# Performance work log

Measured on AMD Instinct MI355X. Metric: run time of the kernel, lower is better.

## Reference

```python
import jax, jax.numpy as jnp
import numpy as np

NF4 = jnp.array([-1.0, -0.6961928009986877, -0.5250730514526367, -0.39491748809814453,
                 -0.28444138169288635, -0.18477343022823334, -0.09105003625154495, 0.0,
                 0.07958029955625534, 0.16093020141124725, 0.24611230194568634,
                 0.33791524171829224, 0.44070982933044434, 0.5626170039176941,
                 0.7229568362236023, 1.0], dtype=jnp.float32)
BLOCK_SIZE = 64
SCALING = 32.0 / 16.0  # alpha / rank


def setup_inputs() -> dict:
    key = jax.random.key(0)
    k = jax.random.split(key, 6)
    B, S, IN, OUT, R = 4, 128, 4096, 11008, 16
    n_blocks = (OUT * IN) // BLOCK_SIZE  # 704512, exact (no padding needed)
    return {
        "x": jax.random.normal(k[0], (B, S, IN), jnp.float32),
        "weight_indices": jax.random.randint(k[1], (OUT, IN), 0, 16, dtype=jnp.int32),
        "weight_scales": jax.random.uniform(k[2], (n_blocks,), jnp.float32),
        "lora_A": jax.random.normal(k[3], (IN, R), jnp.float32),
        "lora_B": jax.random.normal(k[4], (R, OUT), jnp.float32),
        "bias": jax.random.normal(k[5], (OUT,), jnp.float32),
    }


def dequantize_nf4(indices, scales, shape):
    # LUT gather then blockwise absmax scale
    w = NF4[indices.reshape(-1)]                    # [out*in]
    w = w.reshape(-1, BLOCK_SIZE) * scales[:, None]  # [n_blocks, block]
    return w.reshape(shape)                          # [out, in]


def reference(x, weight_indices, weight_scales, lora_A, lora_B, bias):
    W = dequantize_nf4(weight_indices, weight_scales, weight_indices.shape)  # [out, in]
    base = jnp.einsum("bsi,oi->bso", x, W) + bias                            # F.linear
    lora = (x @ lora_A) @ lora_B                                             # low-rank path (dropout p=0 -> identity)
    return base + lora * SCALING
```

## Files before the change

### kernel.cpp

```cpp
#include <hip/hip_runtime.h>
#include <stdint.h>

typedef __bf16 bf16x8 __attribute__((ext_vector_type(8)));
typedef float f32x4 __attribute__((ext_vector_type(4)));
typedef unsigned short ushort_t;

#define N_OUT 11008
#define K_DIM 4096
#define M_DIM 512
#define BM 128
#define BN 64
#define BK 64
#define NT 64
#define LDB 72
#define BUF (64 * LDB)

__constant__ float c_nf4[16] = {
    -1.0f, -0.6961928009986877f, -0.5250730514526367f, -0.39491748809814453f,
    -0.28444138169288635f, -0.18477343022823334f, -0.09105003625154495f, 0.0f,
    0.07958029955625534f, 0.16093020141124725f, 0.24611230194568634f,
    0.33791524171829224f, 0.44070982933044434f, 0.5626170039176941f,
    0.7229568362236023f, 1.0f};

__device__ __forceinline__ uint32_t pkbf(float lo, float hi) {
  uint32_t ul = __builtin_bit_cast(uint32_t, lo);
  uint32_t uh = __builtin_bit_cast(uint32_t, hi);
  return ((ul + 0x8000u) >> 16) | ((uh + 0x8000u) & 0xffff0000u);
}

__device__ __forceinline__ bf16x8 ldfrag(const ushort_t* p) {
  uint4 r = *reinterpret_cast<const uint4*>(p);
  return __builtin_bit_cast(bf16x8, r);
}

__device__ __forceinline__ bf16x8 asfrag(uint4 r) {
  return __builtin_bit_cast(bf16x8, r);
}

__device__ __forceinline__ uint32_t dq2(int a, int b, float s, const float2* lut) {
  float2 l = lut[a | (b << 4)];
  return pkbf(l.x * s, l.y * s);
}

__global__ void k_prep(const float* __restrict__ x, const float* __restrict__ lA,
                       const float* __restrict__ lB, ushort_t* __restrict__ xbf,
                       ushort_t* __restrict__ xap, ushort_t* __restrict__ btp) {
  __shared__ float red[16][17];
  const int b = blockIdx.x, t = threadIdx.x;
  if (b < 1024) {
    int oc = b * 256 + t;
    const float4* s4 = reinterpret_cast<const float4*>(x) + (size_t)oc * 2;
    float4 v0 = s4[0], v1 = s4[1];
    uint4 o;
    o.x = pkbf(v0.x, v0.y);
    o.y = pkbf(v0.z, v0.w);
    o.z = pkbf(v1.x, v1.y);
    o.w = pkbf(v1.z, v1.w);
    ((uint4*)xbf)[oc] = o;
  } else if (b < 1536) {
    int m = b - 1024;
    int r = t & 15, part = t >> 4;
    const float* xr = x + (size_t)m * K_DIM + part * 256;
    const float* ar = lA + (size_t)(part * 256) * 16 + r;
    float acc = 0.f;
#pragma unroll 8
    for (int k = 0; k < 256; ++k) acc += xr[k] * ar[(size_t)k * 16];
    red[part][r] = acc;
    __syncthreads();
    if (t < 32) {
      float v = 0.f;
      if (t < 16) {
        for (int p = 0; p < 16; ++p) v += red[p][t];
        v *= 2.0f;
      }
      uint32_t u = __builtin_bit_cast(uint32_t, v);
      xap[(size_t)m * 32 + t] = (ushort_t)((u + 0x8000u) >> 16);
    }
  } else {
    int o = (b - 1536) * 256 + t;
    uint32_t p[8];
#pragma unroll
    for (int j = 0; j < 8; ++j)
      p[j] = pkbf(lB[(size_t)(2 * j) * N_OUT + o], lB[(size_t)(2 * j + 1) * N_OUT + o]);
    uint4* dst = reinterpret_cast<uint4*>(btp + (size_t)o * 32);
    dst[0] = make_uint4(p[0], p[1], p[2], p[3]);
    dst[1] = make_uint4(p[4], p[5], p[6], p[7]);
    dst[2] = make_uint4(0u, 0u, 0u, 0u);
    dst[3] = make_uint4(0u, 0u, 0u, 0u);
  }
}

__launch_bounds__(256, 3)
__global__ void k_main(const ushort_t* __restrict__ xbf, const int* __restrict__ wi,
                       const float* __restrict__ sc, const ushort_t* __restrict__ xap,
                       const ushort_t* __restrict__ btp, const float* __restrict__ bias,
                       float* __restrict__ out) {
  __shared__ __align__(16) ushort_t lds_b[3 * BUF];
  __shared__ float2 lutp[256];

  const int t = threadIdx.x;
  const int lane = t & 63;
  const int w = t >> 6;
  const int q = lane >> 4;
  const int m0 = blockIdx.x * BM;
  const int o0 = blockIdx.y * BN;

  lutp[t] = make_float2(c_nf4[t & 15], c_nf4[t >> 4]);

  const int brow = t >> 2, bq = t & 3;
  const int* gb = wi + (size_t)(o0 + brow) * K_DIM + bq * 16;
  const float* gs = sc + (size_t)(o0 + brow) * 64;
  const int lbo = brow * LDB + bq * 16;

  const ushort_t* gA = xbf + (size_t)(m0 + w * 32 + (lane & 15)) * K_DIM + q * 8;

  f32x4 acc[2][4];
#pragma unroll
  for (int mi = 0; mi < 2; ++mi)
#pragma unroll
    for (int ni = 0; ni < 4; ++ni) acc[mi][ni] = (f32x4){0.f, 0.f, 0.f, 0.f};

  int4 bi[2][4];
  float bs[2];
  uint4 a_reg[2][2];
#pragma unroll
  for (int j = 0; j < 4; ++j) bi[0][j] = reinterpret_cast<const int4*>(gb)[j];
  bs[0] = gs[0];
#pragma unroll
  for (int j = 0; j < 4; ++j) bi[1][j] = reinterpret_cast<const int4*>(gb + 64)[j];
  bs[1] = gs[1];
#pragma unroll
  for (int mi = 0; mi < 2; ++mi)
#pragma unroll
    for (int kc = 0; kc < 2; ++kc)
      a_reg[mi][kc] =
          *reinterpret_cast<const uint4*>(gA + (size_t)mi * 16 * K_DIM + kc * 32);

  __syncthreads();

  {
    ushort_t* lb = lds_b + lbo;
    uint4 w0, w1;
    w0.x = dq2(bi[0][0].x, bi[0][0].y, bs[0], lutp);
    w0.y = dq2(bi[0][0].z, bi[0][0].w, bs[0], lutp);
    w0.z = dq2(bi[0][1].x, bi[0][1].y, bs[0], lutp);
    w0.w = dq2(bi[0][1].z, bi[0][1].w, bs[0], lutp);
    w1.x = dq2(bi[0][2].x, bi[0][2].y, bs[0], lutp);
    w1.y = dq2(bi[0][2].z, bi[0][2].w, bs[0], lutp);
    w1.z = dq2(bi[0][3].x, bi[0][3].y, bs[0], lutp);
    w1.w = dq2(bi[0][3].z, bi[0][3].w, bs[0], lutp);
    *reinterpret_cast<uint4*>(lb) = w0;
    *reinterpret_cast<uint4*>(lb + 8) = w1;
  }
#pragma unroll
  for (int j = 0; j < 4; ++j) bi[0][j] = reinterpret_cast<const int4*>(gb + 128)[j];
  bs[0] = gs[2];

  unsigned off_r = 0, off_w = BUF, off_s = 2 * BUF;

#pragma unroll 2
  for (int kt = 0; kt < NT; ++kt) {
    __syncthreads();
    const ushort_t* bb = lds_b + off_r + (lane & 15) * LDB + q * 8;
    bf16x8 bv0[4], bv1[4];
#pragma unroll
    for (int ni = 0; ni < 4; ++ni) bv0[ni] = ldfrag(bb + ni * 16 * LDB);
#pragma unroll
    for (int ni = 0; ni < 4; ++ni) bv1[ni] = ldfrag(bb + ni * 16 * LDB + 32);
    const int ns = (kt + 1) & 1;
    if (kt + 1 < NT) {
      ushort_t* lb = lds_b + off_w + lbo;
      uint4 w0, w1;
      w0.x = dq2(bi[ns][0].x, bi[ns][0].y, bs[ns], lutp);
      w0.y = dq2(bi[ns][0].z, bi[ns][0].w, bs[ns], lutp);
      w0.z = dq2(bi[ns][1].x, bi[ns][1].y, bs[ns], lutp);
      w0.w = dq2(bi[ns][1].z, bi[ns][1].w, bs[ns], lutp);
      w1.x = dq2(bi[ns][2].x, bi[ns][2].y, bs[ns], lutp);
      w1.y = dq2(bi[ns][2].z, bi[ns][2].w, bs[ns], lutp);
      w1.z = dq2(bi[ns][3].x, bi[ns][3].y, bs[ns], lutp);
      w1.w = dq2(bi[ns][3].z, bi[ns][3].w, bs[ns], lutp);
      *reinterpret_cast<uint4*>(lb) = w0;
      *reinterpret_cast<uint4*>(lb + 8) = w1;
    }
#pragma unroll
    for (int mi = 0; mi < 2; ++mi)
#pragma unroll
      for (int ni = 0; ni < 4; ++ni)
        acc[mi][ni] = __builtin_amdgcn_mfma_f32_16x16x32_bf16(
            asfrag(a_reg[mi][0]), bv0[ni], acc[mi][ni], 0, 0, 0);
#pragma unroll
    for (int mi = 0; mi < 2; ++mi)
#pragma unroll
      for (int ni = 0; ni < 4; ++ni)
        acc[mi][ni] = __builtin_amdgcn_mfma_f32_16x16x32_bf16(
            asfrag(a_reg[mi][1]), bv1[ni], acc[mi][ni], 0, 0, 0);
    if (kt + 3 < NT) {
      const int4* gp = reinterpret_cast<const int4*>(gb + (size_t)(kt + 3) * 64);
#pragma unroll
      for (int j = 0; j < 4; ++j) bi[ns][j] = gp[j];
      bs[ns] = gs[kt + 3];
    }
    if (kt + 1 < NT) {
#pragma unroll
      for (int mi = 0; mi < 2; ++mi)
#pragma unroll
        for (int kc = 0; kc < 2; ++kc)
          a_reg[mi][kc] = *reinterpret_cast<const uint4*>(
              gA + (size_t)mi * 16 * K_DIM + (size_t)(kt + 1) * 64 + kc * 32);
    }
    unsigned tmp = off_r;
    off_r = off_w;
    off_w = off_s;
    off_s = tmp;
  }

  {
    uint4 la[2], lb4[4];
#pragma unroll
    for (int mi = 0; mi < 2; ++mi)
      la[mi] = *reinterpret_cast<const uint4*>(
          xap + (size_t)(m0 + w * 32 + mi * 16 + (lane & 15)) * 32 + q * 8);
#pragma unroll
    for (int ni = 0; ni < 4; ++ni)
      lb4[ni] = *reinterpret_cast<const uint4*>(
          btp + (size_t)(o0 + ni * 16 + (lane & 15)) * 32 + q * 8);
#pragma unroll
    for (int mi = 0; mi < 2; ++mi)
#pragma unroll
      for (int ni = 0; ni < 4; ++ni)
        acc[mi][ni] = __builtin_amdgcn_mfma_f32_16x16x32_bf16(
            asfrag(la[mi]), asfrag(lb4[ni]), acc[mi][ni], 0, 0, 0);
  }

  const int cl = lane & 15, rg = q * 4;
#pragma unroll
  for (int ni = 0; ni < 4; ++ni) {
    int col = o0 + ni * 16 + cl;
    float bvs = bias[col];
#pragma unroll
    for (int mi = 0; mi < 2; ++mi) {
      int row0 = m0 + w * 32 + mi * 16 + rg;
      float* op = out + (size_t)row0 * N_OUT + col;
#pragma unroll
      for (int i = 0; i < 4; ++i) op[(size_t)i * N_OUT] = acc[mi][ni][i] + bvs;
    }
  }
}

extern "C" void kernel_launch(void* const* d_in, const int* in_sizes, int n_in,
                              void* d_out, int out_size, void* d_ws, size_t ws_size,
                              hipStream_t stream) {
  const float* x = (const float*)d_in[0];
  const int* wi = (const int*)d_in[1];
  const float* sc = (const float*)d_in[2];
  const float* lA = (const float*)d_in[3];
  const float* lB = (const float*)d_in[4];
  const float* bias = (const float*)d_in[5];
  float* out = (float*)d_out;

  char* wsb = (char*)d_ws;
  ushort_t* xbf = (ushort_t*)wsb;
  ushort_t* xap = (ushort_t*)(wsb + (4u << 20));
  ushort_t* btp = (ushort_t*)(wsb + (4u << 20) + (32u << 10));

  k_prep<<<1579, 256, 0, stream>>>(x, lA, lB, xbf, xap, btp);
  dim3 grid(M_DIM / BM, N_OUT / BN);
  k_main<<<grid, 256, 0, stream>>>(xbf, wi, sc, xap, btp, bias, out);
}
```

Measured before the change: 408.9 us.

## Remap grid for XCD L2 reuse and dequantize NF4 with register byte-permutes

Replaces the 2D grid with a 1D grid of 704 blocks remapped so that the four M-tiles sharing a weight column tile land on the same XCD. Those blocks can then share the int32 weight indices in that XCD's L2 instead of each fetching them separately; blocks whose remapped index falls past the last tile exit early. NF4 dequantization no longer reads a float2 pair LUT in LDS. Each thread builds a per-block scaled bf16 table in registers and looks values up with v_perm byte selects. The LDS ring shrinks from triple to double buffering, and B-fragment loads are split into two phases to reduce register pressure. The trade-off is a few idle blocks and more ALU work to build the table at every k-step.

```diff
diff --git a/kernel.cpp b/kernel.cpp
--- a/kernel.cpp
+++ b/kernel.cpp
@@ -37,9 +37,42 @@
   return __builtin_bit_cast(bf16x8, r);
 }
 
-__device__ __forceinline__ uint32_t dq2(int a, int b, float s, const float2* lut) {
-  float2 l = lut[a | (b << 4)];
-  return pkbf(l.x * s, l.y * s);
+struct DQTab {
+  uint32_t thi[4], tlo[4];
+};
+
+__device__ __forceinline__ DQTab build_tab(const float* fl, float s) {
+  DQTab t;
+  uint32_t p[8];
+#pragma unroll
+  for (int j = 0; j < 8; ++j) p[j] = pkbf(fl[2 * j] * s, fl[2 * j + 1] * s);
+#pragma unroll
+  for (int j = 0; j < 4; ++j) {
+    t.thi[j] = __builtin_amdgcn_perm(p[2 * j + 1], p[2 * j], 0x07050301u);
+    t.tlo[j] = __builtin_amdgcn_perm(p[2 * j + 1], p[2 * j], 0x06040200u);
+  }
+  return t;
+}
+
+__device__ __forceinline__ uint32_t pack4(int4 v) {
+  return (uint32_t)v.x | ((uint32_t)v.y << 8) | ((uint32_t)v.z << 16) |
+         ((uint32_t)v.w << 24);
+}
+
+__device__ __forceinline__ uint2 lookup4(uint32_t X, const DQTab& t) {
+  uint32_t selA = X & 0x07070707u;
+  uint32_t m = X & 0x08080808u;
+  uint32_t bsel = 0x03020100u + (m >> 1);
+  uint32_t hA = __builtin_amdgcn_perm(t.thi[1], t.thi[0], selA);
+  uint32_t hB = __builtin_amdgcn_perm(t.thi[3], t.thi[2], selA);
+  uint32_t H = __builtin_amdgcn_perm(hB, hA, bsel);
+  uint32_t lA = __builtin_amdgcn_perm(t.tlo[1], t.tlo[0], selA);
+  uint32_t lB = __builtin_amdgcn_perm(t.tlo[3], t.tlo[2], selA);
+  uint32_t L = __builtin_amdgcn_perm(lB, lA, bsel);
+  uint2 r;
+  r.x = __builtin_amdgcn_perm(H, L, 0x05010400u);
+  r.y = __builtin_amdgcn_perm(H, L, 0x07030602u);
+  return r;
 }
 
 __global__ void k_prep(const float* __restrict__ x, const float* __restrict__ lA,
@@ -95,17 +128,23 @@
                        const float* __restrict__ sc, const ushort_t* __restrict__ xap,
                        const ushort_t* __restrict__ btp, const float* __restrict__ bias,
                        float* __restrict__ out) {
-  __shared__ __align__(16) ushort_t lds_b[3 * BUF];
-  __shared__ float2 lutp[256];
+  __shared__ __align__(16) ushort_t lds_b[2 * BUF];
+
+  const int b = blockIdx.x;
+  const int xcd = b & 7, sl = b >> 3;
+  const int o_idx = xcd * 22 + (sl >> 2);
+  if (o_idx >= 172) return;
+  const int m0 = (sl & 3) * BM;
+  const int o0 = o_idx * BN;
 
   const int t = threadIdx.x;
   const int lane = t & 63;
   const int w = t >> 6;
   const int q = lane >> 4;
-  const int m0 = blockIdx.x * BM;
-  const int o0 = blockIdx.y * BN;
-
-  lutp[t] = make_float2(c_nf4[t & 15], c_nf4[t >> 4]);
+
+  float fl[16];
+#pragma unroll
+  for (int i = 0; i < 16; ++i) fl[i] = c_nf4[i];
 
   const int brow = t >> 2, bq = t & 3;
   const int* gb = wi + (size_t)(o0 + brow) * K_DIM + bq * 16;
@@ -121,14 +160,18 @@
     for (int ni = 0; ni < 4; ++ni) acc[mi][ni] = (f32x4){0.f, 0.f, 0.f, 0.f};
 
   int4 bi[2][4];
-  float bs[2];
+  float bs2[2];
   uint4 a_reg[2][2];
-#pragma unroll
-  for (int j = 0; j < 4; ++j) bi[0][j] = reinterpret_cast<const int4*>(gb)[j];
-  bs[0] = gs[0];
+  int4 b0[4];
+#pragma unroll
+  for (int j = 0; j < 4; ++j) b0[j] = reinterpret_cast<const int4*>(gb)[j];
+  float s0 = gs[0];
 #pragma unroll
   for (int j = 0; j < 4; ++j) bi[1][j] = reinterpret_cast<const int4*>(gb + 64)[j];
-  bs[1] = gs[1];
+  bs2[1] = gs[1];
+#pragma unroll
+  for (int j = 0; j < 4; ++j) bi[0][j] = reinterpret_cast<const int4*>(gb + 128)[j];
+  bs2[0] = gs[2];
 #pragma unroll
   for (int mi = 0; mi < 2; ++mi)
 #pragma unroll
@@ -136,69 +179,59 @@
       a_reg[mi][kc] =
           *reinterpret_cast<const uint4*>(gA + (size_t)mi * 16 * K_DIM + kc * 32);
 
-  __syncthreads();
-
   {
+    DQTab tb = build_tab(fl, s0);
+    uint2 w0 = lookup4(pack4(b0[0]), tb);
+    uint2 w1 = lookup4(pack4(b0[1]), tb);
+    uint2 w2 = lookup4(pack4(b0[2]), tb);
+    uint2 w3 = lookup4(pack4(b0[3]), tb);
     ushort_t* lb = lds_b + lbo;
-    uint4 w0, w1;
-    w0.x = dq2(bi[0][0].x, bi[0][0].y, bs[0], lutp);
-    w0.y = dq2(bi[0][0].z, bi[0][0].w, bs[0], lutp);
-    w0.z = dq2(bi[0][1].x, bi[0][1].y, bs[0], lutp);
-    w0.w = dq2(bi[0][1].z, bi[0][1].w, bs[0], lutp);
-    w1.x = dq2(bi[0][2].x, bi[0][2].y, bs[0], lutp);
-    w1.y = dq2(bi[0][2].z, bi[0][2].w, bs[0], lutp);
-    w1.z = dq2(bi[0][3].x, bi[0][3].y, bs[0], lutp);
-    w1.w = dq2(bi[0][3].z, bi[0][3].w, bs[0], lutp);
-    *reinterpret_cast<uint4*>(lb) = w0;
-    *reinterpret_cast<uint4*>(lb + 8) = w1;
-  }
-#pragma unroll
-  for (int j = 0; j < 4; ++j) bi[0][j] = reinterpret_cast<const int4*>(gb + 128)[j];
-  bs[0] = gs[2];
-
-  unsigned off_r = 0, off_w = BUF, off_s = 2 * BUF;
+    *reinterpret_cast<uint4*>(lb) = make_uint4(w0.x, w0.y, w1.x, w1.y);
+    *reinterpret_cast<uint4*>(lb + 8) = make_uint4(w2.x, w2.y, w3.x, w3.y);
+  }
 
 #pragma unroll 2
   for (int kt = 0; kt < NT; ++kt) {
     __syncthreads();
-    const ushort_t* bb = lds_b + off_r + (lane & 15) * LDB + q * 8;
-    bf16x8 bv0[4], bv1[4];
-#pragma unroll
-    for (int ni = 0; ni < 4; ++ni) bv0[ni] = ldfrag(bb + ni * 16 * LDB);
-#pragma unroll
-    for (int ni = 0; ni < 4; ++ni) bv1[ni] = ldfrag(bb + ni * 16 * LDB + 32);
+    const ushort_t* bb = lds_b + (kt & 1) * BUF + (lane & 15) * LDB + q * 8;
     const int ns = (kt + 1) & 1;
     if (kt + 1 < NT) {
-      ushort_t* lb = lds_b + off_w + lbo;
-      uint4 w0, w1;
-      w0.x = dq2(bi[ns][0].x, bi[ns][0].y, bs[ns], lutp);
-      w0.y = dq2(bi[ns][0].z, bi[ns][0].w, bs[ns], lutp);
-      w0.z = dq2(bi[ns][1].x, bi[ns][1].y, bs[ns], lutp);
-      w0.w = dq2(bi[ns][1].z, bi[ns][1].w, bs[ns], lutp);
-      w1.x = dq2(bi[ns][2].x, bi[ns][2].y, bs[ns], lutp);
-      w1.y = dq2(bi[ns][2].z, bi[ns][2].w, bs[ns], lutp);
-      w1.z = dq2(bi[ns][3].x, bi[ns][3].y, bs[ns], lutp);
-      w1.w = dq2(bi[ns][3].z, bi[ns][3].w, bs[ns], lutp);
-      *reinterpret_cast<uint4*>(lb) = w0;
-      *reinterpret_cast<uint4*>(lb + 8) = w1;
-    }
-#pragma unroll
-    for (int mi = 0; mi < 2; ++mi)
-#pragma unroll
-      for (int ni = 0; ni < 4; ++ni)
-        acc[mi][ni] = __builtin_amdgcn_mfma_f32_16x16x32_bf16(
-            asfrag(a_reg[mi][0]), bv0[ni], acc[mi][ni], 0, 0, 0);
-#pragma unroll
-    for (int mi = 0; mi < 2; ++mi)
-#pragma unroll
-      for (int ni = 0; ni < 4; ++ni)
-        acc[mi][ni] = __builtin_amdgcn_mfma_f32_16x16x32_bf16(
-            asfrag(a_reg[mi][1]), bv1[ni], acc[mi][ni], 0, 0, 0);
+      DQTab tb = build_tab(fl, bs2[ns]);
+      uint2 w0 = lookup4(pack4(bi[ns][0]), tb);
+      uint2 w1 = lookup4(pack4(bi[ns][1]), tb);
+      uint2 w2 = lookup4(pack4(bi[ns][2]), tb);
+      uint2 w3 = lookup4(pack4(bi[ns][3]), tb);
+      ushort_t* lb = lds_b + ns * BUF + lbo;
+      *reinterpret_cast<uint4*>(lb) = make_uint4(w0.x, w0.y, w1.x, w1.y);
+      *reinterpret_cast<uint4*>(lb + 8) = make_uint4(w2.x, w2.y, w3.x, w3.y);
+    }
+    {
+      bf16x8 bv[4];
+#pragma unroll
+      for (int ni = 0; ni < 4; ++ni) bv[ni] = ldfrag(bb + ni * 16 * LDB);
+#pragma unroll
+      for (int mi = 0; mi < 2; ++mi)
+#pragma unroll
+        for (int ni = 0; ni < 4; ++ni)
+          acc[mi][ni] = __builtin_amdgcn_mfma_f32_16x16x32_bf16(
+              asfrag(a_reg[mi][0]), bv[ni], acc[mi][ni], 0, 0, 0);
+    }
+    {
+      bf16x8 bv[4];
+#pragma unroll
+      for (int ni = 0; ni < 4; ++ni) bv[ni] = ldfrag(bb + ni * 16 * LDB + 32);
+#pragma unroll
+      for (int mi = 0; mi < 2; ++mi)
+#pragma unroll
+        for (int ni = 0; ni < 4; ++ni)
+          acc[mi][ni] = __builtin_amdgcn_mfma_f32_16x16x32_bf16(
+              asfrag(a_reg[mi][1]), bv[ni], acc[mi][ni], 0, 0, 0);
+    }
     if (kt + 3 < NT) {
       const int4* gp = reinterpret_cast<const int4*>(gb + (size_t)(kt + 3) * 64);
 #pragma unroll
       for (int j = 0; j < 4; ++j) bi[ns][j] = gp[j];
-      bs[ns] = gs[kt + 3];
+      bs2[ns] = gs[kt + 3];
     }
     if (kt + 1 < NT) {
 #pragma unroll
@@ -208,10 +241,6 @@
           a_reg[mi][kc] = *reinterpret_cast<const uint4*>(
               gA + (size_t)mi * 16 * K_DIM + (size_t)(kt + 1) * 64 + kc * 32);
     }
-    unsigned tmp = off_r;
-    off_r = off_w;
-    off_w = off_s;
-    off_s = tmp;
   }
 
   {
@@ -264,6 +293,5 @@
   ushort_t* btp = (ushort_t*)(wsb + (4u << 20) + (32u << 10));
 
   k_prep<<<1579, 256, 0, stream>>>(x, lA, lB, xbf, xap, btp);
-  dim3 grid(M_DIM / BM, N_OUT / BN);
-  k_main<<<grid, 256, 0, stream>>>(xbf, wi, sc, xap, btp, bias, out);
-}
+  k_main<<<704, 256, 0, stream>>>(xbf, wi, sc, xap, btp, bias, out);
+}
```

After: 391.4 us. 4.3% less time.
